# Kernel tuning notes

Hardware: AMD Instinct MI355X
Metric: run time of the kernel (lower is better)

Reference implementation:

```python
import jax, jax.numpy as jnp
import numpy as np

# DMV constants (direction 0 = child left of head, per `direction = 0 if head_i > child_i`)
NC, HC, GO, STOP, LEFT, RIGHT = 0, 1, 0, 1, 0, 1
NEG = -1e9
B, N, T = 1024, 64, 64


def setup_inputs():
    key = jax.random.key(0)
    ks = jax.random.split(key, 6)
    tag_array = jax.random.randint(ks[0], (B, N), 0, T)
    # valid lengths in [N//2, N]
    len_array = jax.random.randint(ks[1], (B,), N // 2, N + 1)
    id_array = jnp.arange(B, dtype=jnp.int32)
    # parameters are log-probabilities in the original model; normalize for realism
    root_param = jax.nn.log_softmax(0.1 * jax.random.normal(ks[2], (T,), jnp.float32))
    trans_param = jax.nn.log_softmax(0.1 * jax.random.normal(ks[3], (T, T, 2, 1), jnp.float32), axis=1)
    dec_param = jax.nn.log_softmax(0.1 * jax.random.normal(ks[4], (T, 2, 2, 2), jnp.float32), axis=3)
    return dict(id_array=id_array, tag_array=tag_array, len_array=len_array,
                root_param=root_param, trans_param=trans_param, dec_param=dec_param)


def dmv_inside(root_param, trans_param, dec_param, tag_array, len_array):
    """Batched DMV inside algorithm (log space, sum semiring). Returns [B] log-likelihoods."""
    Bs, n = tag_array.shape
    lse = jax.nn.logsumexp
    th = tag_array
    tp = trans_param[..., 0]                                   # [T,T,2] (cv=1)
    trans_l = tp[th[:, :, None], th[:, None, :], LEFT]          # [B,h,m] attach m left of h
    trans_r = tp[th[:, :, None], th[:, None, :], RIGHT]         # [B,h,m] attach m right of h
    dec = dec_param[th]                                         # [B,n,dir,val,decision]
    goR_nc, goR_hc = dec[:, :, RIGHT, NC, GO], dec[:, :, RIGHT, HC, GO]
    goL_nc, goL_hc = dec[:, :, LEFT, NC, GO], dec[:, :, LEFT, HC, GO]
    stR_nc, stR_hc = dec[:, :, RIGHT, NC, STOP], dec[:, :, RIGHT, HC, STOP]
    stL_nc, stL_hc = dec[:, :, LEFT, NC, STOP], dec[:, :, LEFT, HC, STOP]
    root = root_param[th]                                       # [B,n]

    ar = jnp.arange(n)
    full = jnp.full((Bs, n, n), NEG, dtype=trans_r.dtype)
    # C*: half-constituent without STOP; F*: finished half-constituent (with STOP)
    CR = full.at[:, ar, ar].set(0.0)
    CL = full.at[:, ar, ar].set(0.0)
    FR = full.at[:, ar, ar].set(stR_nc)
    FL = full.at[:, ar, ar].set(stL_nc)
    IR = full
    IL = full

    for w in range(1, n):                                       # span width
        k = jnp.arange(w)
        # ---------- right direction: head h, span [h, e=h+w] ----------
        h = jnp.arange(n - w); e = h + w
        S = h[:, None] + k[None, :]                             # split s in [h, e-1]
        go = jnp.where(k[None, None, :] == 0, goR_nc[:, h, None], goR_hc[:, h, None])
        inner = CR[:, h[:, None], S] + go + FL[:, e[:, None], S + 1]
        ir = trans_r[:, h, e] + lse(inner, axis=-1)             # attach e as child of h
        IR = IR.at[:, h, e].set(ir)
        M = S + 1                                               # last child m in [h+1, e]
        cr = lse(IR[:, h[:, None], M] + FR[:, M, e[:, None]], axis=-1)
        CR = CR.at[:, h, e].set(cr)
        FR = FR.at[:, h, e].set(cr + stR_hc[:, h])
        # ---------- left direction: head h, span [m0=h-w, h] ----------
        hl = jnp.arange(w, n); m0 = hl - w
        S2 = hl[:, None] - k[None, :]                           # split s in [m0+1, h]
        go2 = jnp.where(k[None, None, :] == 0, goL_nc[:, hl, None], goL_hc[:, hl, None])
        inner2 = CL[:, hl[:, None], S2] + go2 + FR[:, m0[:, None], S2 - 1]
        il = trans_l[:, hl, m0] + lse(inner2, axis=-1)          # attach m0 as child of h
        IL = IL.at[:, hl, m0].set(il)
        M2 = S2 - 1                                             # last child m in [m0, h-1]
        cl = lse(IL[:, hl[:, None], M2] + FL[:, M2, m0[:, None]], axis=-1)
        CL = CL.at[:, hl, m0].set(cl)
        FL = FL.at[:, hl, m0].set(cl + stL_hc[:, hl])

    # root picks one head r covering [0, len-1]
    last = len_array - 1
    fr_end = FR[jnp.arange(Bs)[:, None], ar[None, :], last[:, None]]   # [B,n]
    score = root + FL[:, :, 0] + fr_end
    score = jnp.where(ar[None, :] < len_array[:, None], score, NEG)
    return lse(score, axis=-1)


def reference(id_array, tag_array, len_array, root_param, trans_param, dec_param):
    # forward() -> per-sentence inside log-probability ('sum' mode since e_step_mode='em')
    return dmv_inside(root_param, trans_param, dec_param, tag_array, len_array)
```

## Files before the change

kernel.cpp:

```cpp
#include <hip/hip_runtime.h>


#define NEGV   -1000000000.0f
#define NMAX   64
#define LDS_S  69
#define BLOCK  512
#define ALPHA  8.0f

#if __has_builtin(__builtin_amdgcn_exp2f)
#define EXP2F(x) __builtin_amdgcn_exp2f(x)
#else
#define EXP2F(x) __expf((x) * 0.6931471805599453f)
#endif
#if __has_builtin(__builtin_amdgcn_logf)
#define LOG2F(x) __builtin_amdgcn_logf(x)
#else
#define LOG2F(x) (__logf(x) * 1.4426950408889634f)
#endif
#define LOG2E 1.4426950408889634f
#define LN2   0.6931471805599453f

template<int CTRL>
__device__ __forceinline__ float dppf(float v) {
    return __int_as_float(__builtin_amdgcn_update_dpp(
        0, __float_as_int(v), CTRL, 0xF, 0xF, true));
}
__device__ __forceinline__ float grp4_sum(float s) {
    s += dppf<0xB1>(s);
    s += dppf<0x4E>(s);
    return s;
}

__device__ __forceinline__ void lse_merge(float& m, float& s, float mo, float so) {
    float mn = fmaxf(m, mo);
    s = s * EXP2F(m - mn) + so * EXP2F(mo - mn);
    m = mn;
}

__global__ void order_kernel(const int* __restrict__ len_arr,
                             int* __restrict__ blk2item, int B)
{
    __shared__ int hist[33];
    __shared__ int base[33];
    const int tid = threadIdx.x;
    if (tid < 33) hist[tid] = 0;
    __syncthreads();
    int bin = 0;
    if (tid < B) {
        bin = 64 - len_arr[tid];
        atomicAdd(&hist[bin], 1);
    }
    __syncthreads();
    if (tid == 0) {
        int acc = 0;
        for (int i = 0; i < 33; ++i) { base[i] = acc; acc += hist[i]; }
    }
    __syncthreads();
    if (tid < B) {
        int rank = atomicAdd(&base[bin], 1);
        int j;
        if ((B & 255) == 0) {
            int q = rank >> 8, pos = rank & 255;
            j = (q & 1) ? ((q << 8) + 255 - pos) : ((q << 8) + pos);
        } else {
            j = rank;
        }
        blk2item[j] = tid;
    }
}

template<int NJ>
__device__ __forceinline__ void dmv_step(
    const int w, const int cd, const int gid, const int lg,
    float* __restrict__ sI, float* __restrict__ sF,
    const float* __restrict__ goNC, const float* __restrict__ goHM,
    const float* __restrict__ stHC, const float* __restrict__ stNC,
    const int* __restrict__ th_s, const float* __restrict__ trans_param)
{
    const int cells = 2 * cd;
    if (gid >= cells) return;
    const bool isR = gid < cd;
    const int  sd  = isR ? 1 : 0;
    const int  h   = isR ? gid : (w + gid - cd);
    const int  e   = isR ? (h + w) : (h - w);

    const float tr  = trans_param[(th_s[h] * NMAX + th_s[e]) * 2 + sd] * LOG2E
                      + ALPHA;
    const float gnc = goNC[sd * NMAX + h];
    const float ghm = goHM[sd * NMAX + h];
    const float dcO = stNC[(sd ^ 1) * NMAX + e];
    const int   kG  = isR ? 0 : (w - 1);
    const int   kD  = isR ? (w - 1) : 0;
    const int   pF  = h * LDS_S + (isR ? h : (h - w + 1));
    const int   pC  = e * LDS_S + (isR ? (h + 1) : e);
    float x[NJ];
    #pragma unroll
    for (int j = 0; j < NJ; ++j) {
        const int k = lg + 4 * j;
        if (j == NJ - 1) {
            const int kc = (k < w) ? k : (w - 1);
            float vF = sF[pF + kc];
            float vC = sF[pC + kc];
            float v = ((k == kG) ? gnc : (vF + ghm)) + ((k == kD) ? dcO : vC);
            x[j] = (k < w) ? v : NEGV;
        } else if (j == 0) {
            float vF = sF[pF + k];
            float vC = sF[pC + k];
            x[j] = ((k == kG) ? gnc : (vF + ghm)) + ((k == kD) ? dcO : vC);
        } else {
            x[j] = (sF[pF + k] + ghm) + sF[pC + k];
        }
    }
    float sA = 0.f;
    #pragma unroll
    for (int j = 0; j < NJ; ++j) sA += EXP2F(x[j]);
    sA = grp4_sum(sA);
    const float ir = LOG2F(sA) + tr;
    if (lg == 0) sI[h * LDS_S + e] = ir;

    const float dcN = stNC[sd * NMAX + e];
    const float sth = stHC[sd * NMAX + h];
    const int   kS  = isR ? (w - 1) : 0;
    const int   pI  = h * LDS_S + (isR ? (h + 1) : e);
    const int   pG  = (isR ? (h + 1) : e) * LDS_S + e;
    float y[NJ];
    #pragma unroll
    for (int j = 0; j < NJ; ++j) {
        const int k = lg + 4 * j;
        if (j == NJ - 1) {
            const int kc = (k < w) ? k : (w - 1);
            float i1 = sI[pI + kc];
            float f1 = sF[pG + kc * LDS_S];
            float v = ((k == kS) ? ir : i1) + ((k == kS) ? dcN : f1);
            y[j] = (k < w) ? v : NEGV;
        } else if (j == 0) {
            float i1 = sI[pI + k];
            float f1 = sF[pG + k * LDS_S];
            y[j] = ((k == kS) ? ir : i1) + ((k == kS) ? dcN : f1);
        } else {
            y[j] = sI[pI + k] + sF[pG + k * LDS_S];
        }
    }
    float sB = 0.f;
    #pragma unroll
    for (int j = 0; j < NJ; ++j) sB += EXP2F(y[j]);
    sB = grp4_sum(sB);
    if (lg == 0) sF[h * LDS_S + e] = LOG2F(sB) + sth;
}

__global__ __launch_bounds__(BLOCK, 8)
void dmv_inside_kernel(const int* __restrict__ tag,
                       const int* __restrict__ len_arr,
                       const float* __restrict__ root_param,
                       const float* __restrict__ trans_param,
                       const float* __restrict__ dec_param,
                       const int* __restrict__ blk2item,
                       float* __restrict__ out)
{
    __shared__ float sI[NMAX * LDS_S];
    __shared__ float sF[NMAX * LDS_S];
    __shared__ float goNC[2 * NMAX];
    __shared__ float goHM[2 * NMAX];
    __shared__ float stHC[2 * NMAX];
    __shared__ float stNC[2 * NMAX];
    __shared__ float root_s[NMAX];
    __shared__ int   th_s[NMAX];

    const int b   = blk2item[blockIdx.x];
    const int tid = threadIdx.x;
    const int nl  = len_arr[b];

    if (tid < NMAX) {
        int t = tag[b * NMAX + tid];
        th_s[tid] = t;
        const float* d = dec_param + t * 8;
        goNC[0 * NMAX + tid] = d[0] * LOG2E;
        stNC[0 * NMAX + tid] = d[1] * LOG2E;
        goHM[0 * NMAX + tid] = (d[2] - d[3]) * LOG2E;
        stHC[0 * NMAX + tid] = d[3] * LOG2E;
        goNC[1 * NMAX + tid] = d[4] * LOG2E;
        stNC[1 * NMAX + tid] = d[5] * LOG2E;
        goHM[1 * NMAX + tid] = (d[6] - d[7]) * LOG2E;
        stHC[1 * NMAX + tid] = d[7] * LOG2E;
        root_s[tid]          = root_param[t] * LOG2E;
    }
    __syncthreads();

    const int gid = tid >> 2;
    const int lg  = tid & 3;

    for (int w = 1; w < nl; ++w) {
        const int cd = nl - w;
        switch ((w - 1) >> 2) {
        case  0: dmv_step< 1>(w, cd, gid, lg, sI, sF, goNC, goHM, stHC, stNC, th_s, trans_param); break;
        case  1: dmv_step< 2>(w, cd, gid, lg, sI, sF, goNC, goHM, stHC, stNC, th_s, trans_param); break;
        case  2: dmv_step< 3>(w, cd, gid, lg, sI, sF, goNC, goHM, stHC, stNC, th_s, trans_param); break;
        case  3: dmv_step< 4>(w, cd, gid, lg, sI, sF, goNC, goHM, stHC, stNC, th_s, trans_param); break;
        case  4: dmv_step< 5>(w, cd, gid, lg, sI, sF, goNC, goHM, stHC, stNC, th_s, trans_param); break;
        case  5: dmv_step< 6>(w, cd, gid, lg, sI, sF, goNC, goHM, stHC, stNC, th_s, trans_param); break;
        case  6: dmv_step< 7>(w, cd, gid, lg, sI, sF, goNC, goHM, stHC, stNC, th_s, trans_param); break;
        case  7: dmv_step< 8>(w, cd, gid, lg, sI, sF, goNC, goHM, stHC, stNC, th_s, trans_param); break;
        case  8: dmv_step< 9>(w, cd, gid, lg, sI, sF, goNC, goHM, stHC, stNC, th_s, trans_param); break;
        case  9: dmv_step<10>(w, cd, gid, lg, sI, sF, goNC, goHM, stHC, stNC, th_s, trans_param); break;
        case 10: dmv_step<11>(w, cd, gid, lg, sI, sF, goNC, goHM, stHC, stNC, th_s, trans_param); break;
        case 11: dmv_step<12>(w, cd, gid, lg, sI, sF, goNC, goHM, stHC, stNC, th_s, trans_param); break;
        case 12: dmv_step<13>(w, cd, gid, lg, sI, sF, goNC, goHM, stHC, stNC, th_s, trans_param); break;
        case 13: dmv_step<14>(w, cd, gid, lg, sI, sF, goNC, goHM, stHC, stNC, th_s, trans_param); break;
        case 14: dmv_step<15>(w, cd, gid, lg, sI, sF, goNC, goHM, stHC, stNC, th_s, trans_param); break;
        default: dmv_step<16>(w, cd, gid, lg, sI, sF, goNC, goHM, stHC, stNC, th_s, trans_param); break;
        }
        __syncthreads();
    }

    if (tid < 64) {
        const int last = nl - 1;
        float fl0 = (tid == 0)    ? stNC[0 * NMAX + 0]    : sF[tid * LDS_S + 0];
        float fre = (tid == last) ? stNC[1 * NMAX + last] : sF[tid * LDS_S + last];
        float xx  = (tid < nl) ? (root_s[tid] + fl0 + fre) : NEGV;
        float m = xx, s = 1.0f;
        #pragma unroll
        for (int off = 1; off < 64; off <<= 1)
            lse_merge(m, s, __shfl_xor(m, off, 64), __shfl_xor(s, off, 64));
        if (tid == 0) out[b] = (m + LOG2F(s) - ALPHA * last) * LN2;
    }
}

extern "C" void kernel_launch(void* const* d_in, const int* in_sizes, int n_in,
                              void* d_out, int out_size, void* d_ws, size_t ws_size,
                              hipStream_t stream) {
    const int*   tag   = (const int*)d_in[1];
    const int*   len_a = (const int*)d_in[2];
    const float* root  = (const float*)d_in[3];
    const float* trans = (const float*)d_in[4];
    const float* dec   = (const float*)d_in[5];
    float* outp = (float*)d_out;
    const int B = in_sizes[2];

    int* blk2item = (int*)d_ws;

    int sortThreads = (B < 1024) ? ((B + 63) & ~63) : 1024;
    if (sortThreads < 64) sortThreads = 64;
    order_kernel<<<1, sortThreads, 0, stream>>>(len_a, blk2item, B);
    dmv_inside_kernel<<<B, BLOCK, 0, stream>>>(tag, len_a, root, trans, dec,
                                               blk2item, outp);
}
```

Baseline: 61.73 us.

## Switch inside-algorithm recurrences from log space to scaled linear space

The DP tables now hold probabilities in linear space instead of log space. The per-span logsumexp, with an exp2 per term and a log2 per cell, becomes an FMA dot product plus a multiply. A per-span scale of 2^ALPHA is folded into the transition weight to limit underflow, and it is removed at the root with a single log. This cuts most transcendental instructions from the inner loops but relies on the fixed scale keeping values inside fp32 range, which risks underflow or overflow on other parameter distributions.

New measurement: 57.60 us. 6.7% less time.

```diff
diff --git a/kernel.cpp b/kernel.cpp
--- a/kernel.cpp
+++ b/kernel.cpp
@@ -31,12 +31,6 @@
     return s;
 }
 
-__device__ __forceinline__ void lse_merge(float& m, float& s, float mo, float so) {
-    float mn = fmaxf(m, mo);
-    s = s * EXP2F(m - mn) + so * EXP2F(mo - mn);
-    m = mn;
-}
-
 __global__ void order_kernel(const int* __restrict__ len_arr,
                              int* __restrict__ blk2item, int B)
 {
@@ -73,8 +67,8 @@
 __device__ __forceinline__ void dmv_step(
     const int w, const int cd, const int gid, const int lg,
     float* __restrict__ sI, float* __restrict__ sF,
-    const float* __restrict__ goNC, const float* __restrict__ goHM,
-    const float* __restrict__ stHC, const float* __restrict__ stNC,
+    const float* __restrict__ goNCl, const float* __restrict__ goHMl,
+    const float* __restrict__ stHCl, const float* __restrict__ stNCl,
     const int* __restrict__ th_s, const float* __restrict__ trans_param)
 {
     const int cells = 2 * cd;
@@ -84,16 +78,16 @@
     const int  h   = isR ? gid : (w + gid - cd);
     const int  e   = isR ? (h + w) : (h - w);
 
-    const float tr  = trans_param[(th_s[h] * NMAX + th_s[e]) * 2 + sd] * LOG2E
-                      + ALPHA;
-    const float gnc = goNC[sd * NMAX + h];
-    const float ghm = goHM[sd * NMAX + h];
-    const float dcO = stNC[(sd ^ 1) * NMAX + e];
+    const float trl = EXP2F(trans_param[(th_s[h] * NMAX + th_s[e]) * 2 + sd]
+                            * LOG2E + ALPHA);
+    const float gnc = goNCl[sd * NMAX + h];
+    const float gm  = goHMl[sd * NMAX + h];
+    const float dcO = stNCl[(sd ^ 1) * NMAX + e];
     const int   kG  = isR ? 0 : (w - 1);
     const int   kD  = isR ? (w - 1) : 0;
     const int   pF  = h * LDS_S + (isR ? h : (h - w + 1));
     const int   pC  = e * LDS_S + (isR ? (h + 1) : e);
-    float x[NJ];
+    float sInt = 0.f, sBnd = 0.f;
     #pragma unroll
     for (int j = 0; j < NJ; ++j) {
         const int k = lg + 4 * j;
@@ -101,29 +95,26 @@
             const int kc = (k < w) ? k : (w - 1);
             float vF = sF[pF + kc];
             float vC = sF[pC + kc];
-            float v = ((k == kG) ? gnc : (vF + ghm)) + ((k == kD) ? dcO : vC);
-            x[j] = (k < w) ? v : NEGV;
+            float v  = ((k == kG) ? gnc : (vF * gm)) * ((k == kD) ? dcO : vC);
+            sBnd += (k < w) ? v : 0.f;
         } else if (j == 0) {
             float vF = sF[pF + k];
             float vC = sF[pC + k];
-            x[j] = ((k == kG) ? gnc : (vF + ghm)) + ((k == kD) ? dcO : vC);
+            sBnd += ((k == kG) ? gnc : (vF * gm)) * ((k == kD) ? dcO : vC);
         } else {
-            x[j] = (sF[pF + k] + ghm) + sF[pC + k];
-        }
-    }
-    float sA = 0.f;
-    #pragma unroll
-    for (int j = 0; j < NJ; ++j) sA += EXP2F(x[j]);
-    sA = grp4_sum(sA);
-    const float ir = LOG2F(sA) + tr;
+            sInt = fmaf(sF[pF + k], sF[pC + k], sInt);
+        }
+    }
+    float sA = grp4_sum(fmaf(gm, sInt, sBnd));
+    const float ir = trl * sA;
     if (lg == 0) sI[h * LDS_S + e] = ir;
 
-    const float dcN = stNC[sd * NMAX + e];
-    const float sth = stHC[sd * NMAX + h];
-    const int   kS  = isR ? (w - 1) : 0;
-    const int   pI  = h * LDS_S + (isR ? (h + 1) : e);
-    const int   pG  = (isR ? (h + 1) : e) * LDS_S + e;
-    float y[NJ];
+    const float dcN  = stNCl[sd * NMAX + e];
+    const float sthl = stHCl[sd * NMAX + h];
+    const int   kS   = isR ? (w - 1) : 0;
+    const int   pI   = h * LDS_S + (isR ? (h + 1) : e);
+    const int   pG   = (isR ? (h + 1) : e) * LDS_S + e;
+    float tInt = 0.f, tBnd = 0.f;
     #pragma unroll
     for (int j = 0; j < NJ; ++j) {
         const int k = lg + 4 * j;
@@ -131,21 +122,18 @@
             const int kc = (k < w) ? k : (w - 1);
             float i1 = sI[pI + kc];
             float f1 = sF[pG + kc * LDS_S];
-            float v = ((k == kS) ? ir : i1) + ((k == kS) ? dcN : f1);
-            y[j] = (k < w) ? v : NEGV;
+            float v  = ((k == kS) ? ir : i1) * ((k == kS) ? dcN : f1);
+            tBnd += (k < w) ? v : 0.f;
         } else if (j == 0) {
             float i1 = sI[pI + k];
             float f1 = sF[pG + k * LDS_S];
-            y[j] = ((k == kS) ? ir : i1) + ((k == kS) ? dcN : f1);
+            tBnd += ((k == kS) ? ir : i1) * ((k == kS) ? dcN : f1);
         } else {
-            y[j] = sI[pI + k] + sF[pG + k * LDS_S];
-        }
-    }
-    float sB = 0.f;
-    #pragma unroll
-    for (int j = 0; j < NJ; ++j) sB += EXP2F(y[j]);
-    sB = grp4_sum(sB);
-    if (lg == 0) sF[h * LDS_S + e] = LOG2F(sB) + sth;
+            tInt = fmaf(sI[pI + k], sF[pG + k * LDS_S], tInt);
+        }
+    }
+    float sB = grp4_sum(tInt + tBnd);
+    if (lg == 0) sF[h * LDS_S + e] = sthl * sB;
 }
 
 __global__ __launch_bounds__(BLOCK, 8)
@@ -159,11 +147,11 @@
 {
     __shared__ float sI[NMAX * LDS_S];
     __shared__ float sF[NMAX * LDS_S];
-    __shared__ float goNC[2 * NMAX];
-    __shared__ float goHM[2 * NMAX];
-    __shared__ float stHC[2 * NMAX];
-    __shared__ float stNC[2 * NMAX];
-    __shared__ float root_s[NMAX];
+    __shared__ float goNCl[2 * NMAX];
+    __shared__ float goHMl[2 * NMAX];
+    __shared__ float stHCl[2 * NMAX];
+    __shared__ float stNCl[2 * NMAX];
+    __shared__ float root_l[NMAX];
     __shared__ int   th_s[NMAX];
 
     const int b   = blk2item[blockIdx.x];
@@ -174,15 +162,15 @@
         int t = tag[b * NMAX + tid];
         th_s[tid] = t;
         const float* d = dec_param + t * 8;
-        goNC[0 * NMAX + tid] = d[0] * LOG2E;
-        stNC[0 * NMAX + tid] = d[1] * LOG2E;
-        goHM[0 * NMAX + tid] = (d[2] - d[3]) * LOG2E;
-        stHC[0 * NMAX + tid] = d[3] * LOG2E;
-        goNC[1 * NMAX + tid] = d[4] * LOG2E;
-        stNC[1 * NMAX + tid] = d[5] * LOG2E;
-        goHM[1 * NMAX + tid] = (d[6] - d[7]) * LOG2E;
-        stHC[1 * NMAX + tid] = d[7] * LOG2E;
-        root_s[tid]          = root_param[t] * LOG2E;
+        goNCl[0 * NMAX + tid] = EXP2F(d[0] * LOG2E);
+        stNCl[0 * NMAX + tid] = EXP2F(d[1] * LOG2E);
+        goHMl[0 * NMAX + tid] = EXP2F((d[2] - d[3]) * LOG2E);
+        stHCl[0 * NMAX + tid] = EXP2F(d[3] * LOG2E);
+        goNCl[1 * NMAX + tid] = EXP2F(d[4] * LOG2E);
+        stNCl[1 * NMAX + tid] = EXP2F(d[5] * LOG2E);
+        goHMl[1 * NMAX + tid] = EXP2F((d[6] - d[7]) * LOG2E);
+        stHCl[1 * NMAX + tid] = EXP2F(d[7] * LOG2E);
+        root_l[tid]           = EXP2F(root_param[t] * LOG2E);
     }
     __syncthreads();
 
@@ -192,36 +180,35 @@
     for (int w = 1; w < nl; ++w) {
         const int cd = nl - w;
         switch ((w - 1) >> 2) {
-        case  0: dmv_step< 1>(w, cd, gid, lg, sI, sF, goNC, goHM, stHC, stNC, th_s, trans_param); break;
-        case  1: dmv_step< 2>(w, cd, gid, lg, sI, sF, goNC, goHM, stHC, stNC, th_s, trans_param); break;
-        case  2: dmv_step< 3>(w, cd, gid, lg, sI, sF, goNC, goHM, stHC, stNC, th_s, trans_param); break;
-        case  3: dmv_step< 4>(w, cd, gid, lg, sI, sF, goNC, goHM, stHC, stNC, th_s, trans_param); break;
-        case  4: dmv_step< 5>(w, cd, gid, lg, sI, sF, goNC, goHM, stHC, stNC, th_s, trans_param); break;
-        case  5: dmv_step< 6>(w, cd, gid, lg, sI, sF, goNC, goHM, stHC, stNC, th_s, trans_param); break;
-        case  6: dmv_step< 7>(w, cd, gid, lg, sI, sF, goNC, goHM, stHC, stNC, th_s, trans_param); break;
-        case  7: dmv_step< 8>(w, cd, gid, lg, sI, sF, goNC, goHM, stHC, stNC, th_s, trans_param); break;
-        case  8: dmv_step< 9>(w, cd, gid, lg, sI, sF, goNC, goHM, stHC, stNC, th_s, trans_param); break;
-        case  9: dmv_step<10>(w, cd, gid, lg, sI, sF, goNC, goHM, stHC, stNC, th_s, trans_param); break;
-        case 10: dmv_step<11>(w, cd, gid, lg, sI, sF, goNC, goHM, stHC, stNC, th_s, trans_param); break;
-        case 11: dmv_step<12>(w, cd, gid, lg, sI, sF, goNC, goHM, stHC, stNC, th_s, trans_param); break;
-        case 12: dmv_step<13>(w, cd, gid, lg, sI, sF, goNC, goHM, stHC, stNC, th_s, trans_param); break;
-        case 13: dmv_step<14>(w, cd, gid, lg, sI, sF, goNC, goHM, stHC, stNC, th_s, trans_param); break;
-        case 14: dmv_step<15>(w, cd, gid, lg, sI, sF, goNC, goHM, stHC, stNC, th_s, trans_param); break;
-        default: dmv_step<16>(w, cd, gid, lg, sI, sF, goNC, goHM, stHC, stNC, th_s, trans_param); break;
+        case  0: dmv_step< 1>(w, cd, gid, lg, sI, sF, goNCl, goHMl, stHCl, stNCl, th_s, trans_param); break;
+        case  1: dmv_step< 2>(w, cd, gid, lg, sI, sF, goNCl, goHMl, stHCl, stNCl, th_s, trans_param); break;
+        case  2: dmv_step< 3>(w, cd, gid, lg, sI, sF, goNCl, goHMl, stHCl, stNCl, th_s, trans_param); break;
+        case  3: dmv_step< 4>(w, cd, gid, lg, sI, sF, goNCl, goHMl, stHCl, stNCl, th_s, trans_param); break;
+        case  4: dmv_step< 5>(w, cd, gid, lg, sI, sF, goNCl, goHMl, stHCl, stNCl, th_s, trans_param); break;
+        case  5: dmv_step< 6>(w, cd, gid, lg, sI, sF, goNCl, goHMl, stHCl, stNCl, th_s, trans_param); break;
+        case  6: dmv_step< 7>(w, cd, gid, lg, sI, sF, goNCl, goHMl, stHCl, stNCl, th_s, trans_param); break;
+        case  7: dmv_step< 8>(w, cd, gid, lg, sI, sF, goNCl, goHMl, stHCl, stNCl, th_s, trans_param); break;
+        case  8: dmv_step< 9>(w, cd, gid, lg, sI, sF, goNCl, goHMl, stHCl, stNCl, th_s, trans_param); break;
+        case  9: dmv_step<10>(w, cd, gid, lg, sI, sF, goNCl, goHMl, stHCl, stNCl, th_s, trans_param); break;
+        case 10: dmv_step<11>(w, cd, gid, lg, sI, sF, goNCl, goHMl, stHCl, stNCl, th_s, trans_param); break;
+        case 11: dmv_step<12>(w, cd, gid, lg, sI, sF, goNCl, goHMl, stHCl, stNCl, th_s, trans_param); break;
+        case 12: dmv_step<13>(w, cd, gid, lg, sI, sF, goNCl, goHMl, stHCl, stNCl, th_s, trans_param); break;
+        case 13: dmv_step<14>(w, cd, gid, lg, sI, sF, goNCl, goHMl, stHCl, stNCl, th_s, trans_param); break;
+        case 14: dmv_step<15>(w, cd, gid, lg, sI, sF, goNCl, goHMl, stHCl, stNCl, th_s, trans_param); break;
+        default: dmv_step<16>(w, cd, gid, lg, sI, sF, goNCl, goHMl, stHCl, stNCl, th_s, trans_param); break;
         }
         __syncthreads();
     }
 
     if (tid < 64) {
         const int last = nl - 1;
-        float fl0 = (tid == 0)    ? stNC[0 * NMAX + 0]    : sF[tid * LDS_S + 0];
-        float fre = (tid == last) ? stNC[1 * NMAX + last] : sF[tid * LDS_S + last];
-        float xx  = (tid < nl) ? (root_s[tid] + fl0 + fre) : NEGV;
-        float m = xx, s = 1.0f;
+        float fl0 = (tid == 0)    ? stNCl[0 * NMAX + 0]    : sF[tid * LDS_S + 0];
+        float fre = (tid == last) ? stNCl[1 * NMAX + last] : sF[tid * LDS_S + last];
+        float xx  = (tid < nl) ? (root_l[tid] * fl0 * fre) : 0.f;
         #pragma unroll
         for (int off = 1; off < 64; off <<= 1)
-            lse_merge(m, s, __shfl_xor(m, off, 64), __shfl_xor(s, off, 64));
-        if (tid == 0) out[b] = (m + LOG2F(s) - ALPHA * last) * LN2;
+            xx += __shfl_xor(xx, off, 64);
+        if (tid == 0) out[b] = (LOG2F(xx) - ALPHA * last) * LN2;
     }
 }
 
```
